# Performance work log

Measured on AMD Instinct MI355X. Metric: run time of the kernel, lower is better.

The kernel has to match this reference:

```python
import jax, jax.numpy as jnp
import numpy as np

ALPHA = 0.2  # LeakyReLU negative slope (init arg alpha)


def setup_inputs() -> dict:
    key = jax.random.key(0)
    k1, k2, k3 = jax.random.split(key, 3)
    B, N, F_in, F_out = 8, 2048, 256, 256
    inp = jax.random.normal(k1, (B, N, F_in), dtype=jnp.float32)
    adj = jnp.ones((B, N, N), dtype=jnp.float32)  # unused by the module's forward
    # xavier_uniform with gain=1.414
    gain = 1.414
    bW = gain * np.sqrt(6.0 / (F_in + F_out))
    W = jax.random.uniform(k2, (F_in, F_out), minval=-bW, maxval=bW, dtype=jnp.float32)
    ba = gain * np.sqrt(6.0 / (2 * F_out + 1))
    a = jax.random.uniform(k3, (2 * F_out, 1), minval=-ba, maxval=ba, dtype=jnp.float32)
    return {"inp": inp, "adj": adj, "W": W, "a": a}


def reference(inp, adj, W, a):
    # inp: [B, N, F_in]; W: [F_in, F_out]; a: [2*F_out, 1]. adj is unused (as in source).
    F_out = W.shape[1]
    h = jnp.matmul(inp, W)  # [B, N, F_out]
    # e[b,i,j] = leakyrelu(a1 . h_i + a2 . h_j)  (equivalent to the repeat+cat+matmul)
    a1 = a[:F_out, 0]
    a2 = a[F_out:, 0]
    s1 = jnp.einsum('bnf,f->bn', h, a1)  # [B, N]
    s2 = jnp.einsum('bnf,f->bn', h, a2)  # [B, N]
    e = jax.nn.leaky_relu(s1[:, :, None] + s2[:, None, :], negative_slope=ALPHA)  # [B, N, N]
    # global per-batch min-max normalization, then affine *30 - 20
    mn = jnp.min(e, axis=(1, 2), keepdims=True)
    mx = jnp.max(e, axis=(1, 2), keepdims=True)
    e = (e - mn) / (mx - mn) * 30.0 - 20.0
    attention = jax.nn.sigmoid(e)  # dropout p=0 / eval: identity
    h_prime = jnp.matmul(attention, h)  # [B, N, F_out]
    h_prime = jax.nn.elu(h_prime)  # concat=True branch
    return h_prime, attention
```

## Files before the change

### kernel.cpp

```cpp
#include <hip/hip_runtime.h>
#include <stdint.h>

#define B_   8
#define N_   2048
#define F_   256
#define BN_  (B_ * N_)
#define ALPHA_ 0.2f

typedef __attribute__((ext_vector_type(8))) short  short8;
typedef __attribute__((ext_vector_type(4))) float  f32x4;

__device__ __forceinline__ unsigned short f2bf(float x) {
  uint32_t u = __float_as_uint(x);
  uint32_t r = (u + 0x7fffu + ((u >> 16) & 1u)) >> 16;
  return (unsigned short)r;
}

__device__ __forceinline__ void async_load16(const void* g, void* l) {
  __builtin_amdgcn_global_load_lds(
      (const __attribute__((address_space(1))) uint32_t*)g,
      (__attribute__((address_space(3))) uint32_t*)l, 16, 0, 0);
}

__global__ void k_cvt_inp(const float* __restrict__ x, unsigned short* __restrict__ y) {
  int idx = (blockIdx.x * 256 + threadIdx.x) * 4;
  float4 v = *(const float4*)(x + idx);
  ushort4 p;
  p.x = f2bf(v.x); p.y = f2bf(v.y); p.z = f2bf(v.z); p.w = f2bf(v.w);
  *(ushort4*)(y + idx) = p;
}

__global__ void k_cvt_w(const float* __restrict__ W, unsigned short* __restrict__ WT) {
  int k = blockIdx.x, n = threadIdx.x;
  WT[n * F_ + k] = f2bf(W[k * F_ + n]);
}

__launch_bounds__(256, 1)
__global__ void k_gemm1(const unsigned short* __restrict__ inpb,
                        const unsigned short* __restrict__ WT,
                        const float* __restrict__ avec,
                        unsigned short* __restrict__ hT,
                        float* __restrict__ s1g, float* __restrict__ s2g) {
  __shared__ __align__(16) unsigned short Atile[64 * 32];
  __shared__ __align__(16) unsigned short Btile[256 * 32];
  __shared__ __align__(16) unsigned short Trans[256 * 72];
  __shared__ float s1_lds[64], s2_lds[64];

  const int tid  = threadIdx.x;
  const int wave = tid >> 6, lane = tid & 63;
  const int n16  = lane & 15, quad = lane >> 4;
  const int i0   = blockIdx.x * 64;

  if (tid < 64) { s1_lds[tid] = 0.0f; s2_lds[tid] = 0.0f; }

  f32x4 acc[4][4];
  #pragma unroll
  for (int mt = 0; mt < 4; ++mt)
    #pragma unroll
    for (int nt = 0; nt < 4; ++nt) acc[mt][nt] = (f32x4){0.f, 0.f, 0.f, 0.f};

  for (int k0 = 0; k0 < F_; k0 += 32) {
    {
      int r = (wave << 4) + (lane >> 2);
      int p = lane & 3;
      async_load16(inpb + (size_t)(i0 + r) * F_ + k0 + p * 8,
                   (char*)Atile + wave * 1024);
    }
    #pragma unroll
    for (int g4 = 0; g4 < 4; ++g4) {
      int f = (wave << 6) + (g4 << 4) + (lane >> 2);
      int p = lane & 3;
      async_load16(WT + (size_t)f * F_ + k0 + p * 8,
                   (char*)Btile + wave * 4096 + g4 * 1024);
    }
    __syncthreads();

    short8 af[4], bf_[4];
    #pragma unroll
    for (int mt = 0; mt < 4; ++mt)
      af[mt] = *(const short8*)((const char*)Atile + ((mt * 16 + n16) * 64 + quad * 16));
    #pragma unroll
    for (int nt = 0; nt < 4; ++nt)
      bf_[nt] = *(const short8*)((const char*)Btile + ((wave * 64 + nt * 16 + n16) * 64 + quad * 16));
    #pragma unroll
    for (int mt = 0; mt < 4; ++mt)
      #pragma unroll
      for (int nt = 0; nt < 4; ++nt)
        acc[mt][nt] = __builtin_amdgcn_mfma_f32_16x16x32_bf16(af[mt], bf_[nt], acc[mt][nt], 0, 0, 0);
    __syncthreads();
  }

  #pragma unroll
  for (int mt = 0; mt < 4; ++mt)
    #pragma unroll
    for (int nt = 0; nt < 4; ++nt) {
      int f = (wave << 6) + (nt << 4) + n16;
      int i = (mt << 4) + (quad << 2);
      ushort4 pk;
      pk.x = f2bf(acc[mt][nt][0]); pk.y = f2bf(acc[mt][nt][1]);
      pk.z = f2bf(acc[mt][nt][2]); pk.w = f2bf(acc[mt][nt][3]);
      *(ushort4*)(Trans + f * 72 + i) = pk;
    }

  float a1v[4], a2v[4];
  #pragma unroll
  for (int nt = 0; nt < 4; ++nt) {
    int f = (wave << 6) + (nt << 4) + n16;
    a1v[nt] = avec[f];
    a2v[nt] = avec[F_ + f];
  }
  #pragma unroll
  for (int mt = 0; mt < 4; ++mt) {
    float s1p[4] = {0, 0, 0, 0}, s2p[4] = {0, 0, 0, 0};
    #pragma unroll
    for (int nt = 0; nt < 4; ++nt)
      #pragma unroll
      for (int rg = 0; rg < 4; ++rg) {
        s1p[rg] = fmaf(acc[mt][nt][rg], a1v[nt], s1p[rg]);
        s2p[rg] = fmaf(acc[mt][nt][rg], a2v[nt], s2p[rg]);
      }
    #pragma unroll
    for (int rg = 0; rg < 4; ++rg) {
      float v1 = s1p[rg], v2 = s2p[rg];
      #pragma unroll
      for (int off = 1; off < 16; off <<= 1) {
        v1 += __shfl_xor(v1, off);
        v2 += __shfl_xor(v2, off);
      }
      if (n16 == 0) {
        atomicAdd(&s1_lds[(mt << 4) + (quad << 2) + rg], v1);
        atomicAdd(&s2_lds[(mt << 4) + (quad << 2) + rg], v2);
      }
    }
  }
  __syncthreads();

  #pragma unroll
  for (int it = 0; it < 8; ++it) {
    int f = it * 32 + wave * 8 + (lane >> 3);
    int i = (lane & 7) * 8;
    short8 v = *(const short8*)(Trans + f * 72 + i);
    *(short8*)(hT + (size_t)f * BN_ + i0 + i) = v;
  }
  if (tid < 64) {
    s1g[i0 + tid] = s1_lds[tid];
    s2g[i0 + tid] = s2_lds[tid];
  }
}

__global__ void k_minmax(const float* __restrict__ s1, const float* __restrict__ s2,
                         float2* __restrict__ params) {
  int b = blockIdx.x, tid = threadIdx.x;
  float mn1 = 1e30f, mx1 = -1e30f, mn2 = 1e30f, mx2 = -1e30f;
  for (int i = tid; i < N_; i += 256) {
    float v1 = s1[b * N_ + i]; mn1 = fminf(mn1, v1); mx1 = fmaxf(mx1, v1);
    float v2 = s2[b * N_ + i]; mn2 = fminf(mn2, v2); mx2 = fmaxf(mx2, v2);
  }
  #pragma unroll
  for (int off = 1; off < 64; off <<= 1) {
    mn1 = fminf(mn1, __shfl_xor(mn1, off));
    mx1 = fmaxf(mx1, __shfl_xor(mx1, off));
    mn2 = fminf(mn2, __shfl_xor(mn2, off));
    mx2 = fmaxf(mx2, __shfl_xor(mx2, off));
  }
  __shared__ float red[4][4];
  int wave = tid >> 6, lane = tid & 63;
  if (lane == 0) { red[wave][0] = mn1; red[wave][1] = mx1; red[wave][2] = mn2; red[wave][3] = mx2; }
  __syncthreads();
  if (tid == 0) {
    for (int w = 1; w < 4; ++w) {
      mn1 = fminf(mn1, red[w][0]); mx1 = fmaxf(mx1, red[w][1]);
      mn2 = fminf(mn2, red[w][2]); mx2 = fmaxf(mx2, red[w][3]);
    }
    float smn = mn1 + mn2, smx = mx1 + mx2;
    float mn = fmaxf(smn, ALPHA_ * smn);
    float mx = fmaxf(smx, ALPHA_ * smx);
    float scale = 30.0f / (mx - mn);
    float bias  = -mn * scale - 20.0f;
    params[b] = make_float2(-scale, -bias);
  }
}

__launch_bounds__(256, 2)
__global__ void k_gemm2(const unsigned short* __restrict__ hT,
                        const float* __restrict__ s1, const float* __restrict__ s2,
                        const float2* __restrict__ params,
                        float* __restrict__ hprime,
                        float* __restrict__ att) {
  __shared__ __align__(16) unsigned short Atile[32 * 32];
  __shared__ __align__(16) unsigned short Btile[256 * 32];

  const int tid  = threadIdx.x;
  const int wave = tid >> 6, lane = tid & 63;
  const int n16  = lane & 15, quad = lane >> 4;
  const int blk  = blockIdx.x;
  const int b    = blk & 7;
  const int i0   = (blk >> 3) * 32;

  const float2 pb = params[b];
  const float uscale = pb.x, ubias = pb.y;

  const int r_att = tid >> 3;
  const int c_att = tid & 7;
  const float s1v = s1[b * N_ + i0 + r_att];
  const float* s2b = s2 + b * N_;
  float* attrow = att + ((size_t)(b * N_ + i0 + r_att)) * N_;

  f32x4 acc[2][4];
  #pragma unroll
  for (int mt = 0; mt < 2; ++mt)
    #pragma unroll
    for (int nt = 0; nt < 4; ++nt) acc[mt][nt] = (f32x4){0.f, 0.f, 0.f, 0.f};

  for (int k0 = 0; k0 < N_; k0 += 32) {
    #pragma unroll
    for (int g4 = 0; g4 < 4; ++g4) {
      int f = (wave << 6) + (g4 << 4) + (lane >> 2);
      int p = lane & 3;
      async_load16(hT + (size_t)f * BN_ + b * N_ + k0 + p * 8,
                   (char*)Btile + wave * 4096 + g4 * 1024);
    }

    float4 va = *(const float4*)(s2b + k0 + c_att * 4);
    float v[4] = {va.x, va.y, va.z, va.w};
    ushort4 spk;
    #pragma unroll
    for (int jj = 0; jj < 4; ++jj) {
      float s = s1v + v[jj];
      float l = fmaxf(s, ALPHA_ * s);
      float u = fmaf(l, uscale, ubias);
      float p_ = __builtin_amdgcn_rcpf(1.0f + __expf(u));
      v[jj] = p_;
    }
    spk.x = f2bf(v[0]); spk.y = f2bf(v[1]); spk.z = f2bf(v[2]); spk.w = f2bf(v[3]);
    *(float4*)(attrow + k0 + c_att * 4) = make_float4(v[0], v[1], v[2], v[3]);
    *(ushort4*)(Atile + tid * 4) = spk;
    __syncthreads();

    short8 af[2], bf_[4];
    #pragma unroll
    for (int mt = 0; mt < 2; ++mt)
      af[mt] = *(const short8*)((const char*)Atile + ((mt * 16 + n16) * 64 + quad * 16));
    #pragma unroll
    for (int nt = 0; nt < 4; ++nt)
      bf_[nt] = *(const short8*)((const char*)Btile + ((wave * 64 + nt * 16 + n16) * 64 + quad * 16));
    #pragma unroll
    for (int mt = 0; mt < 2; ++mt)
      #pragma unroll
      for (int nt = 0; nt < 4; ++nt)
        acc[mt][nt] = __builtin_amdgcn_mfma_f32_16x16x32_bf16(af[mt], bf_[nt], acc[mt][nt], 0, 0, 0);
    __syncthreads();
  }

  float* hp = hprime + ((size_t)(b * N_ + i0)) * F_;
  #pragma unroll
  for (int mt = 0; mt < 2; ++mt)
    #pragma unroll
    for (int nt = 0; nt < 4; ++nt) {
      int fcol = (wave << 6) + (nt << 4) + n16;
      int irow = (mt << 4) + (quad << 2);
      #pragma unroll
      for (int rg = 0; rg < 4; ++rg) {
        float x = acc[mt][nt][rg];
        float y = x > 0.0f ? x : (__expf(x) - 1.0f);
        hp[(size_t)(irow + rg) * F_ + fcol] = y;
      }
    }
}

extern "C" void kernel_launch(void* const* d_in, const int* in_sizes, int n_in,
                              void* d_out, int out_size, void* d_ws, size_t ws_size,
                              hipStream_t stream) {
  const float* inp  = (const float*)d_in[0];
  const float* W    = (const float*)d_in[2];
  const float* avec = (const float*)d_in[3];

  float* hprime = (float*)d_out;
  float* att    = (float*)d_out + (size_t)B_ * N_ * F_;

  char* ws = (char*)d_ws;
  unsigned short* inpb = (unsigned short*)ws;
  unsigned short* WT   = (unsigned short*)(ws + 8388608);
  unsigned short* hT   = (unsigned short*)(ws + 8388608 + 131072);
  float* s1            = (float*)(ws + 8388608 + 131072 + 8388608);
  float* s2            = s1 + BN_;
  float2* params       = (float2*)(s2 + BN_);

  k_cvt_inp<<<(BN_ * F_) / 1024, 256, 0, stream>>>(inp, inpb);
  k_cvt_w<<<F_, F_, 0, stream>>>(W, WT);
  k_gemm1<<<BN_ / 64, 256, 0, stream>>>(inpb, WT, avec, hT, s1, s2);
  k_minmax<<<B_, 256, 0, stream>>>(s1, s2, params);
  k_gemm2<<<512, 256, 0, stream>>>(hT, s1, s2, params, hprime, att);
}
```

Measured before the change: 289.3 us.

## Fuse input bf16 conversion and min-max reduction into gemm1, add nontemporal stores

Removes the separate fp32-to-bf16 input conversion kernel by having gemm1 load fp32 rows and convert them in registers before writing LDS. It also removes the min-max kernel: each gemm1 block reduces its s1/s2 values and publishes them through order-preserving integer atomics, and gemm2 computes scale and bias from those keys. The large attention and h_prime outputs are written with nontemporal stores to limit cache pollution. This costs two small memsets per call and gives up async global-to-LDS loads for the A tile in gemm1.

```diff
diff --git a/kernel.cpp b/kernel.cpp
--- a/kernel.cpp
+++ b/kernel.cpp
@@ -16,18 +16,23 @@
   return (unsigned short)r;
 }
 
+__device__ __forceinline__ uint32_t fkey(float f) {
+  uint32_t b = __float_as_uint(f);
+  return b ^ (uint32_t)(((int32_t)b >> 31) | (int32_t)0x80000000);
+}
+__device__ __forceinline__ float ikey(uint32_t k) {
+  uint32_t b = (k & 0x80000000u) ? (k ^ 0x80000000u) : ~k;
+  return __uint_as_float(b);
+}
+
 __device__ __forceinline__ void async_load16(const void* g, void* l) {
   __builtin_amdgcn_global_load_lds(
       (const __attribute__((address_space(1))) uint32_t*)g,
       (__attribute__((address_space(3))) uint32_t*)l, 16, 0, 0);
 }
 
-__global__ void k_cvt_inp(const float* __restrict__ x, unsigned short* __restrict__ y) {
-  int idx = (blockIdx.x * 256 + threadIdx.x) * 4;
-  float4 v = *(const float4*)(x + idx);
-  ushort4 p;
-  p.x = f2bf(v.x); p.y = f2bf(v.y); p.z = f2bf(v.z); p.w = f2bf(v.w);
-  *(ushort4*)(y + idx) = p;
+__device__ __forceinline__ void nt_store4(float* p, f32x4 v) {
+  __builtin_nontemporal_store(v, (f32x4*)p);
 }
 
 __global__ void k_cvt_w(const float* __restrict__ W, unsigned short* __restrict__ WT) {
@@ -36,11 +41,12 @@
 }
 
 __launch_bounds__(256, 1)
-__global__ void k_gemm1(const unsigned short* __restrict__ inpb,
+__global__ void k_gemm1(const float* __restrict__ inp,
                         const unsigned short* __restrict__ WT,
                         const float* __restrict__ avec,
                         unsigned short* __restrict__ hT,
-                        float* __restrict__ s1g, float* __restrict__ s2g) {
+                        float* __restrict__ s1g, float* __restrict__ s2g,
+                        uint32_t* __restrict__ maxk, uint32_t* __restrict__ mink) {
   __shared__ __align__(16) unsigned short Atile[64 * 32];
   __shared__ __align__(16) unsigned short Btile[256 * 32];
   __shared__ __align__(16) unsigned short Trans[256 * 72];
@@ -50,6 +56,7 @@
   const int wave = tid >> 6, lane = tid & 63;
   const int n16  = lane & 15, quad = lane >> 4;
   const int i0   = blockIdx.x * 64;
+  const int b    = i0 >> 11;
 
   if (tid < 64) { s1_lds[tid] = 0.0f; s2_lds[tid] = 0.0f; }
 
@@ -61,10 +68,16 @@
 
   for (int k0 = 0; k0 < F_; k0 += 32) {
     {
-      int r = (wave << 4) + (lane >> 2);
-      int p = lane & 3;
-      async_load16(inpb + (size_t)(i0 + r) * F_ + k0 + p * 8,
-                   (char*)Atile + wave * 1024);
+      int r = tid >> 2, cp = tid & 3;
+      const float* gp = inp + (size_t)(i0 + r) * F_ + k0 + cp * 8;
+      float4 va = *(const float4*)gp;
+      float4 vb = *(const float4*)(gp + 4);
+      short8 sv;
+      sv[0] = (short)f2bf(va.x); sv[1] = (short)f2bf(va.y);
+      sv[2] = (short)f2bf(va.z); sv[3] = (short)f2bf(va.w);
+      sv[4] = (short)f2bf(vb.x); sv[5] = (short)f2bf(vb.y);
+      sv[6] = (short)f2bf(vb.z); sv[7] = (short)f2bf(vb.w);
+      *(short8*)((char*)Atile + r * 64 + cp * 16) = sv;
     }
     #pragma unroll
     for (int g4 = 0; g4 < 4; ++g4) {
@@ -142,49 +155,32 @@
     short8 v = *(const short8*)(Trans + f * 72 + i);
     *(short8*)(hT + (size_t)f * BN_ + i0 + i) = v;
   }
+
   if (tid < 64) {
-    s1g[i0 + tid] = s1_lds[tid];
-    s2g[i0 + tid] = s2_lds[tid];
-  }
-}
-
-__global__ void k_minmax(const float* __restrict__ s1, const float* __restrict__ s2,
-                         float2* __restrict__ params) {
-  int b = blockIdx.x, tid = threadIdx.x;
-  float mn1 = 1e30f, mx1 = -1e30f, mn2 = 1e30f, mx2 = -1e30f;
-  for (int i = tid; i < N_; i += 256) {
-    float v1 = s1[b * N_ + i]; mn1 = fminf(mn1, v1); mx1 = fmaxf(mx1, v1);
-    float v2 = s2[b * N_ + i]; mn2 = fminf(mn2, v2); mx2 = fmaxf(mx2, v2);
-  }
-  #pragma unroll
-  for (int off = 1; off < 64; off <<= 1) {
-    mn1 = fminf(mn1, __shfl_xor(mn1, off));
-    mx1 = fmaxf(mx1, __shfl_xor(mx1, off));
-    mn2 = fminf(mn2, __shfl_xor(mn2, off));
-    mx2 = fmaxf(mx2, __shfl_xor(mx2, off));
-  }
-  __shared__ float red[4][4];
-  int wave = tid >> 6, lane = tid & 63;
-  if (lane == 0) { red[wave][0] = mn1; red[wave][1] = mx1; red[wave][2] = mn2; red[wave][3] = mx2; }
-  __syncthreads();
-  if (tid == 0) {
-    for (int w = 1; w < 4; ++w) {
-      mn1 = fminf(mn1, red[w][0]); mx1 = fmaxf(mx1, red[w][1]);
-      mn2 = fminf(mn2, red[w][2]); mx2 = fmaxf(mx2, red[w][3]);
-    }
-    float smn = mn1 + mn2, smx = mx1 + mx2;
-    float mn = fmaxf(smn, ALPHA_ * smn);
-    float mx = fmaxf(smx, ALPHA_ * smx);
-    float scale = 30.0f / (mx - mn);
-    float bias  = -mn * scale - 20.0f;
-    params[b] = make_float2(-scale, -bias);
+    float v1 = s1_lds[tid], v2 = s2_lds[tid];
+    s1g[i0 + tid] = v1;
+    s2g[i0 + tid] = v2;
+    float mn1 = v1, mx1 = v1, mn2 = v2, mx2 = v2;
+    #pragma unroll
+    for (int off = 1; off < 64; off <<= 1) {
+      mn1 = fminf(mn1, __shfl_xor(mn1, off));
+      mx1 = fmaxf(mx1, __shfl_xor(mx1, off));
+      mn2 = fminf(mn2, __shfl_xor(mn2, off));
+      mx2 = fmaxf(mx2, __shfl_xor(mx2, off));
+    }
+    if (tid == 0) {
+      atomicMax(&maxk[b * 2 + 0], fkey(mx1));
+      atomicMax(&maxk[b * 2 + 1], fkey(mx2));
+      atomicMin(&mink[b * 2 + 0], fkey(mn1));
+      atomicMin(&mink[b * 2 + 1], fkey(mn2));
+    }
   }
 }
 
 __launch_bounds__(256, 2)
 __global__ void k_gemm2(const unsigned short* __restrict__ hT,
                         const float* __restrict__ s1, const float* __restrict__ s2,
-                        const float2* __restrict__ params,
+                        const uint32_t* __restrict__ maxk, const uint32_t* __restrict__ mink,
                         float* __restrict__ hprime,
                         float* __restrict__ att) {
   __shared__ __align__(16) unsigned short Atile[32 * 32];
@@ -197,8 +193,14 @@
   const int b    = blk & 7;
   const int i0   = (blk >> 3) * 32;
 
-  const float2 pb = params[b];
-  const float uscale = pb.x, ubias = pb.y;
+  float mx1 = ikey(maxk[b * 2 + 0]), mx2 = ikey(maxk[b * 2 + 1]);
+  float mn1 = ikey(mink[b * 2 + 0]), mn2 = ikey(mink[b * 2 + 1]);
+  float smn = mn1 + mn2, smx = mx1 + mx2;
+  float emn = fmaxf(smn, ALPHA_ * smn);
+  float emx = fmaxf(smx, ALPHA_ * smx);
+  float scale  = 30.0f / (emx - emn);
+  const float uscale = -scale;
+  const float ubias  = emn * scale + 20.0f;
 
   const int r_att = tid >> 3;
   const int c_att = tid & 7;
@@ -233,7 +235,7 @@
       v[jj] = p_;
     }
     spk.x = f2bf(v[0]); spk.y = f2bf(v[1]); spk.z = f2bf(v[2]); spk.w = f2bf(v[3]);
-    *(float4*)(attrow + k0 + c_att * 4) = make_float4(v[0], v[1], v[2], v[3]);
+    nt_store4(attrow + k0 + c_att * 4, (f32x4){v[0], v[1], v[2], v[3]});
     *(ushort4*)(Atile + tid * 4) = spk;
     __syncthreads();
 
@@ -263,7 +265,7 @@
       for (int rg = 0; rg < 4; ++rg) {
         float x = acc[mt][nt][rg];
         float y = x > 0.0f ? x : (__expf(x) - 1.0f);
-        hp[(size_t)(irow + rg) * F_ + fcol] = y;
+        __builtin_nontemporal_store(y, hp + (size_t)(irow + rg) * F_ + fcol);
       }
     }
 }
@@ -279,16 +281,17 @@
   float* att    = (float*)d_out + (size_t)B_ * N_ * F_;
 
   char* ws = (char*)d_ws;
-  unsigned short* inpb = (unsigned short*)ws;
-  unsigned short* WT   = (unsigned short*)(ws + 8388608);
-  unsigned short* hT   = (unsigned short*)(ws + 8388608 + 131072);
-  float* s1            = (float*)(ws + 8388608 + 131072 + 8388608);
-  float* s2            = s1 + BN_;
-  float2* params       = (float2*)(s2 + BN_);
-
-  k_cvt_inp<<<(BN_ * F_) / 1024, 256, 0, stream>>>(inp, inpb);
+  unsigned short* WT = (unsigned short*)ws;
+  unsigned short* hT = (unsigned short*)(ws + 131072);
+  float* s1          = (float*)(ws + 131072 + 8388608);
+  float* s2          = s1 + BN_;
+  uint32_t* maxk     = (uint32_t*)(s2 + BN_);
+  uint32_t* mink     = maxk + 16;
+
+  (void)hipMemsetAsync(maxk, 0x00, 64, stream);
+  (void)hipMemsetAsync(mink, 0xFF, 64, stream);
+
   k_cvt_w<<<F_, F_, 0, stream>>>(W, WT);
-  k_gemm1<<<BN_ / 64, 256, 0, stream>>>(inpb, WT, avec, hT, s1, s2);
-  k_minmax<<<B_, 256, 0, stream>>>(s1, s2, params);
-  k_gemm2<<<512, 256, 0, stream>>>(hT, s1, s2, params, hprime, att);
-}
+  k_gemm1<<<BN_ / 64, 256, 0, stream>>>(inp, WT, avec, hT, s1, s2, maxk, mink);
+  k_gemm2<<<512, 256, 0, stream>>>(hT, s1, s2, maxk, mink, hprime, att);
+}
```

Result: faster. 281.6 us (-2.7%).
